# Kernel tuning notes

Hardware: AMD Instinct MI355X
Metric: run time of the kernel (lower is better)

## Reference

```python
import jax, jax.numpy as jnp
import numpy as np

MAX_ANGLES = 6
SCALES = 2
BN_EPS = 1e-5


def _gauss(k):
    # Gaussian filter init used by WaveletTransform1D (kernel_size k, sigma=k/4)
    xs = np.arange(k, dtype=np.float32) - k // 2
    w = np.exp(-xs ** 2 / (2.0 * (k / 4.0) ** 2)).astype(np.float32)
    return jnp.asarray((w / w.sum()).reshape(1, 1, k))


def setup_inputs():
    key = jax.random.key(0)
    ks = jax.random.split(key, 8)
    B, C, H, W = 8, 64, 128, 128
    return {
        "x": jax.random.normal(ks[0], (B, C, H, W), jnp.float32),
        "lin1_w": jax.random.normal(ks[1], (32, C * 16), jnp.float32) * 0.02,
        "lin1_b": jnp.zeros((32,), jnp.float32),
        "lin2_w": jax.random.normal(ks[2], (MAX_ANGLES, 32), jnp.float32) * 0.02,
        "lin2_b": jnp.zeros((MAX_ANGLES,), jnp.float32),
        "wf0": _gauss(3),
        "wf1": _gauss(5),
        "fuse_w": jax.random.normal(ks[3], (C, C * SCALES), jnp.float32) * 0.05,
        "fuse_b": jax.random.normal(ks[4], (C,), jnp.float32) * 0.05,
        "bn_gamma": jnp.ones((C,), jnp.float32),
        "bn_beta": jnp.zeros((C,), jnp.float32),
        "bn_mean": jnp.zeros((C,), jnp.float32),
        "bn_var": jnp.ones((C,), jnp.float32),
    }


def _grid_sample(img, grid):
    # torch F.grid_sample, bilinear, align_corners=True, padding_mode='zeros'
    N, C, H, W = img.shape
    ix = (grid[..., 0] + 1.0) * 0.5 * (W - 1)  # (N,Hg,Wg)
    iy = (grid[..., 1] + 1.0) * 0.5 * (H - 1)
    x0 = jnp.floor(ix)
    y0 = jnp.floor(iy)
    wx = ix - x0
    wy = iy - y0

    def gather(xi, yi):
        valid = (xi >= 0) & (xi <= W - 1) & (yi >= 0) & (yi <= H - 1)
        xc = jnp.clip(xi, 0, W - 1).astype(jnp.int32)
        yc = jnp.clip(yi, 0, H - 1).astype(jnp.int32)
        v = jax.vmap(lambda im, yy, xx: im[:, yy, xx])(img, yc, xc)  # (N,C,Hg,Wg)
        return v * valid[:, None, :, :].astype(img.dtype)

    v00 = gather(x0, y0)
    v01 = gather(x0 + 1, y0)
    v10 = gather(x0, y0 + 1)
    v11 = gather(x0 + 1, y0 + 1)
    return (v00 * ((1 - wx) * (1 - wy))[:, None]
            + v01 * (wx * (1 - wy))[:, None]
            + v10 * ((1 - wx) * wy)[:, None]
            + v11 * (wx * wy)[:, None])


def _interp1d(x, Lout):
    # F.interpolate mode='linear', align_corners=False, over last axis
    Lin = x.shape[-1]
    real = jnp.clip((jnp.arange(Lout, dtype=jnp.float32) + 0.5) * (Lin / Lout) - 0.5, 0.0, Lin - 1.0)
    i0 = jnp.floor(real).astype(jnp.int32)
    i1 = jnp.minimum(i0 + 1, Lin - 1)
    w = real - i0
    return x[..., i0] * (1.0 - w) + x[..., i1] * w


def _interp_last_ac(x, Lout):
    # linear interp over last axis, align_corners=True
    Lin = x.shape[-1]
    if Lin == Lout:
        return x
    pos = jnp.arange(Lout, dtype=jnp.float32) * ((Lin - 1) / (Lout - 1))
    i0 = jnp.floor(pos).astype(jnp.int32)
    i1 = jnp.minimum(i0 + 1, Lin - 1)
    w = pos - i0
    return x[..., i0] * (1.0 - w) + x[..., i1] * w


def _avgpool1(x):
    L = x.shape[-1]
    return x[..., : (L // 2) * 2].reshape(x.shape[:-1] + (L // 2, 2)).mean(-1)


def _conv1(sig, w):
    # sig (N,1,L), w (1,1,k), 'same' padding cross-correlation (matches torch Conv1d)
    k = w.shape[-1]
    return jax.lax.conv_general_dilated(sig, w, (1,), [(k // 2, k // 2)],
                                        dimension_numbers=("NCH", "OIH", "NCH"))


def reference(x, lin1_w, lin1_b, lin2_w, lin2_b, wf0, wf1, fuse_w, fuse_b,
              bn_gamma, bn_beta, bn_mean, bn_var):
    B, C, H, W = x.shape
    K = MAX_ANGLES
    # --- AnglePredictor: adaptive avg pool 4x4 (H,W divisible by 4) + MLP ---
    pooled = x.reshape(B, C, 4, H // 4, 4, W // 4).mean(axis=(3, 5))  # (B,C,4,4)
    feat = pooled.reshape(B, C * 16)
    h = jax.nn.relu(feat @ lin1_w.T + lin1_b)
    off = (h @ lin2_w.T + lin2_b) * 30.0
    base = jnp.linspace(0.0, 180.0, K)
    angles = jnp.sort(jnp.clip(base[None, :] + off, 0.0, 180.0), axis=1)  # (B,K)
    # --- RadonTransform: per-angle rotation grid + grid_sample + sum over W ---
    xs = jnp.linspace(-1.0, 1.0, W)
    ys = jnp.linspace(-1.0, 1.0, H)
    yc, xc = jnp.meshgrid(ys, xs, indexing="ij")
    th = angles * (jnp.pi / 180.0)
    co = jnp.cos(th)[:, :, None, None]
    si = jnp.sin(th)[:, :, None, None]
    gx = xc[None, None] * co + yc[None, None] * si
    gy = -xc[None, None] * si + yc[None, None] * co
    grid = jnp.stack([gx, gy], axis=-1).reshape(B * K, H, W, 2)
    xexp = jnp.broadcast_to(x[:, None], (B, K, C, H, W)).reshape(B * K, C, H, W)
    rotated = _grid_sample(xexp, grid)          # (B*K,C,H,W)
    sig = rotated.sum(axis=3)                   # (B*K,C,H) == sinogram permuted
    # --- WaveletTransform1D (2 scales, L=H=128 > 4) ---
    N = B * K
    c0 = _conv1(sig.reshape(N * C, 1, H), wf0).reshape(N, C, H)
    cur = _avgpool1(sig)                        # (N,C,H//2)
    L2 = H // 2
    f1 = _conv1(cur.reshape(N * C, 1, L2), wf1)
    u1 = _interp1d(_avgpool1(f1), L2).reshape(N, C, L2)
    c1 = _interp1d(u1, H)                       # resized to target length H
    coeffs = jnp.stack([c0, c1], axis=2)        # (N,C,SCALES,H)
    wav = coeffs.reshape(B, K, C, SCALES, H).transpose(0, 2, 4, 3, 1)  # (B,C,H,S,K)
    combined = wav.reshape(B, C * SCALES, H, K)  # matches torch .view on contiguous
    # --- bilinear align_corners=True resize (H,K)->(H,W), separable ---
    combined = _interp_last_ac(combined, W)
    combined = _interp_last_ac(combined.swapaxes(-1, -2), H).swapaxes(-1, -2)
    # --- fusion: 1x1 conv + BatchNorm(eval) + ReLU ---
    out = jnp.einsum("oc,bchw->bohw", fuse_w, combined) + fuse_b[None, :, None, None]
    scale = (bn_gamma / jnp.sqrt(bn_var + BN_EPS))[None, :, None, None]
    out = (out - bn_mean[None, :, None, None]) * scale + bn_beta[None, :, None, None]
    return jax.nn.relu(out)
```

## Files before the change

kernel.cpp:

```cpp
#include <hip/hip_runtime.h>
#include <math.h>

#define BB 8
#define CC 64
#define HH 128
#define WW 128
#define KK 6

#define FEAT_OFF 0
#define TH_OFF   8192
#define COEF_OFF 8256
#define S_OFF    (8256 + 786432)

__global__ __launch_bounds__(256) void k_pool(const float* __restrict__ x,
                                              float* __restrict__ ws) {
    int bc = blockIdx.x;
    int b = bc >> 6, c = bc & 63;
    int t = threadIdx.x;
    __shared__ float pool_l[16];
    if (t < 16) pool_l[t] = 0.f;
    __syncthreads();
    const float4* img4 = (const float4*)(x + (size_t)bc * 16384);
    float acc[4] = {0.f, 0.f, 0.f, 0.f};
    int cb = (t & 31) >> 3;
    #pragma unroll
    for (int r = 0; r < 16; ++r) {
        float4 v = img4[r * 256 + t];
        acc[r >> 2] += (v.x + v.y) + (v.z + v.w);
    }
    #pragma unroll
    for (int rb = 0; rb < 4; ++rb)
        atomicAdd(&pool_l[rb * 4 + cb], acc[rb]);
    __syncthreads();
    if (t < 16)
        ws[FEAT_OFF + b * 1024 + c * 16 + t] = pool_l[t] * (1.0f / 1024.0f);
}

__global__ __launch_bounds__(256) void k_mlp(const float* __restrict__ lin1_w,
                                             const float* __restrict__ lin1_b,
                                             const float* __restrict__ lin2_w,
                                             const float* __restrict__ lin2_b,
                                             float* __restrict__ ws) {
    int b = blockIdx.x;
    int t = threadIdx.x;
    __shared__ float feat_l[1024];
    __shared__ float h_l[32];
    __shared__ float ang_l[6];
    const float* feat = ws + FEAT_OFF + b * 1024;
    for (int i = t; i < 1024; i += 256) feat_l[i] = feat[i];
    __syncthreads();
    int m = t >> 3, part = t & 7;
    const float* wrow = lin1_w + m * 1024 + part * 128;
    const float* frow = feat_l + part * 128;
    float acc = 0.f;
    #pragma unroll 8
    for (int i = 0; i < 128; ++i) acc = fmaf(frow[i], wrow[i], acc);
    acc += __shfl_xor(acc, 1);
    acc += __shfl_xor(acc, 2);
    acc += __shfl_xor(acc, 4);
    if (part == 0) h_l[m] = fmaxf(acc + lin1_b[m], 0.f);
    __syncthreads();
    if (t < 6) {
        float a = lin2_b[t];
        #pragma unroll
        for (int i = 0; i < 32; ++i) a = fmaf(h_l[i], lin2_w[t * 32 + i], a);
        a = 36.0f * (float)t + a * 30.0f;
        ang_l[t] = fminf(fmaxf(a, 0.f), 180.f);
    }
    __syncthreads();
    if (t == 0) {
        float v[6];
        #pragma unroll
        for (int i = 0; i < 6; ++i) v[i] = ang_l[i];
        for (int i = 1; i < 6; ++i) {
            float key = v[i]; int j = i - 1;
            while (j >= 0 && v[j] > key) { v[j + 1] = v[j]; --j; }
            v[j + 1] = key;
        }
        #pragma unroll
        for (int i = 0; i < 6; ++i)
            ws[TH_OFF + b * 6 + i] = v[i] * (3.14159265358979323846f / 180.0f);
    }
}

__global__ __launch_bounds__(256) void k_radon(const float* __restrict__ x,
                                               const float* __restrict__ wf0,
                                               const float* __restrict__ wf1,
                                               float* __restrict__ ws) {
    int bc = blockIdx.x;
    int b = bc >> 6, c = bc & 63;
    int t = threadIdx.x;
    __shared__ float imgp[130 * 130];
    __shared__ float sigl[768];
    __shared__ float co_l[6], si_l[6];

    for (int i = t; i < 130; i += 256) {
        imgp[i] = 0.f;
        imgp[129 * 130 + i] = 0.f;
        imgp[i * 130] = 0.f;
        imgp[i * 130 + 129] = 0.f;
    }
    const float4* src4 = (const float4*)(x + (size_t)bc * 16384);
    for (int i = t; i < 4096; i += 256) {
        float4 v = src4[i];
        float* d = imgp + ((i >> 5) + 1) * 130 + ((i & 31) << 2) + 1;
        d[0] = v.x; d[1] = v.y; d[2] = v.z; d[3] = v.w;
    }
    if (t < 6) {
        float th = ws[TH_OFF + b * 6 + t];
        co_l[t] = cosf(th);
        si_l[t] = sinf(th);
    }
    __syncthreads();

    const float* base = imgp + 131;
    const float LO = -0.9999f, HIA = 127.9999f;

    for (int p = t; p < 768; p += 256) {
        int k = p >> 7, h = p & 127;
        float co = co_l[k], si = si_l[k];
        float yc = fmaf((float)h, 2.0f / 127.0f, -1.0f);
        float ix0 = (fmaf(yc, si, -co) + 1.0f) * 63.5f;
        float iy0 = (fmaf(yc, co,  si) + 1.0f) * 63.5f;

        float ic = 1.0f / co, is = 1.0f / (-si);
        float a1 = (LO - ix0) * ic, a2 = (HIA - ix0) * ic;
        float b1 = (LO - iy0) * is, b2 = (HIA - iy0) * is;
        float wlo = fmaxf(fmaxf(fminf(a1, a2), fminf(b1, b2)), 0.0f);
        float whi = fminf(fminf(fmaxf(a1, a2), fmaxf(b1, b2)), 127.0f);
        int wA = (int)ceilf(wlo);
        int wB = (int)floorf(whi) + 1;
        wA = max(0, min(wA, 128));
        wB = max(wA, min(wB, 128));
        while (wA < wB) {
            float ix = fmaf((float)wA, co, ix0), iy = fmaf((float)wA, -si, iy0);
            if (ix >= LO && ix <= HIA && iy >= LO && iy <= HIA) break;
            ++wA;
        }
        while (wB > wA) {
            float ix = fmaf((float)(wB - 1), co, ix0), iy = fmaf((float)(wB - 1), -si, iy0);
            if (ix >= LO && ix <= HIA && iy >= LO && iy <= HIA) break;
            --wB;
        }

        float acc = 0.f;
        for (int w = wA; w < wB; ++w) {
            float fw = (float)w;
            float ix = fmaf(fw,  co, ix0);
            float iy = fmaf(fw, -si, iy0);
            float xf = floorf(ix), yf = floorf(iy);
            float wx = ix - xf, wy = iy - yf;
            int x0 = (int)xf, y0 = (int)yf;
            const float* q = base + y0 * 130 + x0;
            float v00 = q[0], v01 = q[1];
            float v10 = q[130], v11 = q[131];
            float top = fmaf(wx, v01 - v00, v00);
            float bot = fmaf(wx, v11 - v10, v10);
            acc += fmaf(wy, bot - top, top);
        }
        sigl[p] = acc;
    }
    __syncthreads();

    float* cur = imgp;
    float* f1  = imgp + 384;
    float* p1  = imgp + 768;
    float* u1  = imgp + 960;
    float g0 = wf0[0], g1 = wf0[1], g2 = wf0[2];

    for (int p = t; p < 768; p += 256) {
        int k = p >> 7, h = p & 127;
        const float* s = sigl + k * 128;
        float sm1 = (h > 0)   ? s[h - 1] : 0.f;
        float sp1 = (h < 127) ? s[h + 1] : 0.f;
        float c0 = sm1 * g0 + s[h] * g1 + sp1 * g2;
        ws[COEF_OFF + (((b * 6 + k) * 64 + c) * 2 + 0) * 128 + h] = c0;
    }
    for (int q = t; q < 384; q += 256) {
        int k = q >> 6, l = q & 63;
        cur[q] = (sigl[k * 128 + 2 * l] + sigl[k * 128 + 2 * l + 1]) * 0.5f;
    }
    __syncthreads();

    float w10 = wf1[0], w11 = wf1[1], w12 = wf1[2], w13 = wf1[3], w14 = wf1[4];
    for (int q = t; q < 384; q += 256) {
        int k = q >> 6, l = q & 63;
        const float* cu = cur + k * 64;
        float a = cu[l] * w12;
        a += (l >= 2)  ? cu[l - 2] * w10 : 0.f;
        a += (l >= 1)  ? cu[l - 1] * w11 : 0.f;
        a += (l <= 62) ? cu[l + 1] * w13 : 0.f;
        a += (l <= 61) ? cu[l + 2] * w14 : 0.f;
        f1[q] = a;
    }
    __syncthreads();

    for (int q = t; q < 192; q += 256) {
        int k = q >> 5, m = q & 31;
        p1[q] = (f1[k * 64 + 2 * m] + f1[k * 64 + 2 * m + 1]) * 0.5f;
    }
    __syncthreads();

    for (int q = t; q < 384; q += 256) {
        int k = q >> 6, l = q & 63;
        float real = fminf(fmaxf(0.5f * (float)l - 0.25f, 0.f), 31.f);
        int i0 = (int)real;
        int i1 = min(i0 + 1, 31);
        float wv = real - (float)i0;
        u1[q] = p1[k * 32 + i0] * (1.f - wv) + p1[k * 32 + i1] * wv;
    }
    __syncthreads();

    for (int p = t; p < 768; p += 256) {
        int k = p >> 7, h = p & 127;
        float real = fminf(fmaxf(0.5f * (float)h - 0.25f, 0.f), 63.f);
        int i0 = (int)real;
        int i1 = min(i0 + 1, 63);
        float wv = real - (float)i0;
        float c1 = u1[k * 64 + i0] * (1.f - wv) + u1[k * 64 + i1] * wv;
        ws[COEF_OFF + (((b * 6 + k) * 64 + c) * 2 + 1) * 128 + h] = c1;
    }
}

__global__ __launch_bounds__(256) void k_fuse(const float* __restrict__ fuse_w,
                                              const float* __restrict__ fuse_b,
                                              const float* __restrict__ bn_gamma,
                                              const float* __restrict__ bn_beta,
                                              const float* __restrict__ bn_mean,
                                              const float* __restrict__ bn_var,
                                              float* __restrict__ ws) {
    int blk = blockIdx.x;
    int n = blk >> 2, q = blk & 3;
    int b = n / 6, k = n - b * 6;
    int t = threadIdx.x;
    __shared__ __align__(16) float M[128 * 128];
    __shared__ float w_l[16 * 128];
    const float* coef = ws + COEF_OFF + n * 16384;
    for (int i = t; i < 16384; i += 256) {
        int cc = i >> 8, rem = i & 255, s = rem >> 7, hpos = rem & 127;
        int c2 = 2 * cc + (hpos >> 6);
        int h2 = ((hpos & 63) << 1) | s;
        M[c2 * 128 + h2] = coef[i];
    }
    for (int i = t; i < 2048; i += 256)
        w_l[i] = fuse_w[(q * 16 + (i >> 7)) * 128 + (i & 127)];
    __syncthreads();

    int hg = t & 31;
    int og = t >> 5;
    float acc[2][4];
    #pragma unroll
    for (int oo = 0; oo < 2; ++oo)
        #pragma unroll
        for (int j = 0; j < 4; ++j) acc[oo][j] = 0.f;

    const float* w0 = w_l + (og * 2) * 128;
    const float* w1 = w0 + 128;
    for (int c2 = 0; c2 < 128; ++c2) {
        float4 m4 = *(const float4*)(M + c2 * 128 + (hg << 2));
        float a0 = w0[c2], a1 = w1[c2];
        acc[0][0] = fmaf(a0, m4.x, acc[0][0]);
        acc[0][1] = fmaf(a0, m4.y, acc[0][1]);
        acc[0][2] = fmaf(a0, m4.z, acc[0][2]);
        acc[0][3] = fmaf(a0, m4.w, acc[0][3]);
        acc[1][0] = fmaf(a1, m4.x, acc[1][0]);
        acc[1][1] = fmaf(a1, m4.y, acc[1][1]);
        acc[1][2] = fmaf(a1, m4.z, acc[1][2]);
        acc[1][3] = fmaf(a1, m4.w, acc[1][3]);
    }
    #pragma unroll
    for (int oo = 0; oo < 2; ++oo) {
        int o = q * 16 + og * 2 + oo;
        float scale = bn_gamma[o] * rsqrtf(bn_var[o] + 1e-5f);
        float shift = (fuse_b[o] - bn_mean[o]) * scale + bn_beta[o];
        int basei = ((b * 64 + o) * 128 + hg * 4) * 6 + k;
        #pragma unroll
        for (int j = 0; j < 4; ++j)
            ws[S_OFF + basei + j * 6] = fmaf(acc[oo][j], scale, shift);
    }
}

__global__ __launch_bounds__(256) void k_out(const float* __restrict__ S,
                                             float* __restrict__ out) {
    int idx = blockIdx.x * 256 + threadIdx.x;
    int w = idx & 127;
    int row = idx >> 7;
    float pos = (float)w * (5.0f / 127.0f);
    int i0 = min((int)pos, 5);
    int i1 = min(i0 + 1, 5);
    float tt = pos - (float)i0;
    const float* srow = S + row * 6;
    float val = srow[i0] * (1.f - tt) + srow[i1] * tt;
    out[idx] = fmaxf(val, 0.f);
}

extern "C" void kernel_launch(void* const* d_in, const int* in_sizes, int n_in,
                              void* d_out, int out_size, void* d_ws, size_t ws_size,
                              hipStream_t stream) {
    const float* x        = (const float*)d_in[0];
    const float* lin1_w   = (const float*)d_in[1];
    const float* lin1_b   = (const float*)d_in[2];
    const float* lin2_w   = (const float*)d_in[3];
    const float* lin2_b   = (const float*)d_in[4];
    const float* wf0      = (const float*)d_in[5];
    const float* wf1      = (const float*)d_in[6];
    const float* fuse_w   = (const float*)d_in[7];
    const float* fuse_b   = (const float*)d_in[8];
    const float* bn_gamma = (const float*)d_in[9];
    const float* bn_beta  = (const float*)d_in[10];
    const float* bn_mean  = (const float*)d_in[11];
    const float* bn_var   = (const float*)d_in[12];
    float* ws  = (float*)d_ws;
    float* out = (float*)d_out;

    hipLaunchKernelGGL(k_pool,  dim3(BB * CC), dim3(256), 0, stream, x, ws);
    hipLaunchKernelGGL(k_mlp,   dim3(BB),      dim3(256), 0, stream,
                       lin1_w, lin1_b, lin2_w, lin2_b, ws);
    hipLaunchKernelGGL(k_radon, dim3(BB * CC), dim3(256), 0, stream, x, wf0, wf1, ws);
    hipLaunchKernelGGL(k_fuse,  dim3(BB * KK * 4), dim3(256), 0, stream,
                       fuse_w, fuse_b, bn_gamma, bn_beta, bn_mean, bn_var, ws);
    hipLaunchKernelGGL(k_out,   dim3((BB * CC * HH * WW) / 256), dim3(256), 0, stream,
                       ws + S_OFF, out);
}
```

Before: 183.4 us.

## Add transposed LDS image copy and pick per-angle orientation to reduce bank conflicts

```diff
diff --git a/kernel.cpp b/kernel.cpp
--- a/kernel.cpp
+++ b/kernel.cpp
@@ -11,6 +11,14 @@
 #define TH_OFF   8192
 #define COEF_OFF 8256
 #define S_OFF    (8256 + 786432)
+
+#define STR  136
+#define NROW 132
+#define IMG_SZ (NROW * STR)
+#define N_OFF 0
+#define T_OFF IMG_SZ
+#define SIG_OFF (2 * IMG_SZ)
+#define LDS_TOT (2 * IMG_SZ + 768)
 
 __global__ __launch_bounds__(256) void k_pool(const float* __restrict__ x,
                                               float* __restrict__ ws) {
@@ -83,92 +91,119 @@
     }
 }
 
-__global__ __launch_bounds__(256) void k_radon(const float* __restrict__ x,
+__device__ __forceinline__ int sim_mult(float drift) {
+    unsigned c0 = 0, c1 = 0, c2 = 0, sat = 0;
+    for (int i = 0; i < 64; ++i) {
+        int bk = ((int)floorf(drift * (float)i + 0.5f)) & 31;
+        unsigned m = 1u << bk;
+        unsigned t0 = c0 & m;  c0 ^= m;
+        unsigned t1 = c1 & t0; c1 ^= t0;
+        unsigned t2 = c2 & t1; c2 ^= t1;
+        sat |= t2;
+    }
+    int best = 0;
+    for (int bk = 0; bk < 32; ++bk) {
+        int mm = ((c0 >> bk) & 1) | (((c1 >> bk) & 1) << 1)
+               | (((c2 >> bk) & 1) << 2) | (((sat >> bk) & 1) << 3);
+        best = max(best, mm);
+    }
+    return best;
+}
+
+__global__ __launch_bounds__(384) void k_radon(const float* __restrict__ x,
                                                const float* __restrict__ wf0,
                                                const float* __restrict__ wf1,
                                                float* __restrict__ ws) {
     int bc = blockIdx.x;
     int b = bc >> 6, c = bc & 63;
     int t = threadIdx.x;
-    __shared__ float imgp[130 * 130];
-    __shared__ float sigl[768];
+    __shared__ float S[LDS_TOT];
     __shared__ float co_l[6], si_l[6];
-
-    for (int i = t; i < 130; i += 256) {
-        imgp[i] = 0.f;
-        imgp[129 * 130 + i] = 0.f;
-        imgp[i * 130] = 0.f;
-        imgp[i * 130 + 129] = 0.f;
-    }
+    __shared__ int   sel_l[6];
+
+    for (int i = t; i < IMG_SZ; i += 384) S[N_OFF + i] = 0.f;
+    __syncthreads();
     const float4* src4 = (const float4*)(x + (size_t)bc * 16384);
-    for (int i = t; i < 4096; i += 256) {
+    for (int i = t; i < 4096; i += 384) {
         float4 v = src4[i];
-        float* d = imgp + ((i >> 5) + 1) * 130 + ((i & 31) << 2) + 1;
+        float* d = S + N_OFF + ((i >> 5) + 2) * STR + ((i & 31) << 2) + 2;
         d[0] = v.x; d[1] = v.y; d[2] = v.z; d[3] = v.w;
     }
     if (t < 6) {
         float th = ws[TH_OFF + b * 6 + t];
-        co_l[t] = cosf(th);
-        si_l[t] = sinf(th);
-    }
-    __syncthreads();
-
-    const float* base = imgp + 131;
-    const float LO = -0.9999f, HIA = 127.9999f;
-
-    for (int p = t; p < 768; p += 256) {
+        float co = cosf(th), si = sinf(th);
+        co_l[t] = co; si_l[t] = si;
+        int mN = sim_mult(fmaf(136.f, co, si));
+        int mT = sim_mult(fmaf(136.f, si, co));
+        sel_l[t] = (mT < mN) ? 1 : 0;
+    }
+    __syncthreads();
+    for (int j = t; j < NROW * NROW; j += 384) {
+        int yy = j / NROW, xx = j - yy * NROW;
+        S[T_OFF + xx * STR + yy] = S[N_OFF + yy * STR + xx];
+    }
+    __syncthreads();
+
+    #pragma unroll
+    for (int pass = 0; pass < 2; ++pass) {
+        int p = pass * 384 + t;
         int k = p >> 7, h = p & 127;
         float co = co_l[k], si = si_l[k];
+        int sel = sel_l[k];
         float yc = fmaf((float)h, 2.0f / 127.0f, -1.0f);
         float ix0 = (fmaf(yc, si, -co) + 1.0f) * 63.5f;
         float iy0 = (fmaf(yc, co,  si) + 1.0f) * 63.5f;
-
-        float ic = 1.0f / co, is = 1.0f / (-si);
-        float a1 = (LO - ix0) * ic, a2 = (HIA - ix0) * ic;
-        float b1 = (LO - iy0) * is, b2 = (HIA - iy0) * is;
-        float wlo = fmaxf(fmaxf(fminf(a1, a2), fminf(b1, b2)), 0.0f);
-        float whi = fminf(fminf(fmaxf(a1, a2), fmaxf(b1, b2)), 127.0f);
-        int wA = (int)ceilf(wlo);
-        int wB = (int)floorf(whi) + 1;
-        wA = max(0, min(wA, 128));
-        wB = max(wA, min(wB, 128));
-        while (wA < wB) {
-            float ix = fmaf((float)wA, co, ix0), iy = fmaf((float)wA, -si, iy0);
-            if (ix >= LO && ix <= HIA && iy >= LO && iy <= HIA) break;
-            ++wA;
+        float u0 = sel ? ix0 : iy0;
+        float v0 = sel ? iy0 : ix0;
+        float du = sel ? co  : -si;
+        float dv = sel ? -si : co;
+        int abase = (sel ? T_OFF : N_OFF) + 2 * STR + 2;
+
+        float idu = 1.0f / du, idv = 1.0f / dv;
+        float a1 = (-1.0f - u0) * idu, a2 = (128.0f - u0) * idu;
+        float b1 = (-1.0f - v0) * idv, b2 = (128.0f - v0) * idv;
+        float wlo = fmaxf(fminf(a1, a2), fminf(b1, b2));
+        float whi = fminf(fmaxf(a1, a2), fmaxf(b1, b2));
+        int wAl = min(max((int)floorf(wlo), 0), 128);
+        int wBl = min(max((int)ceilf(whi), 0), 127);
+        #pragma unroll
+        for (int sft = 1; sft < 64; sft <<= 1) {
+            wAl = min(wAl, __shfl_xor(wAl, sft));
+            wBl = max(wBl, __shfl_xor(wBl, sft));
         }
-        while (wB > wA) {
-            float ix = fmaf((float)(wB - 1), co, ix0), iy = fmaf((float)(wB - 1), -si, iy0);
-            if (ix >= LO && ix <= HIA && iy >= LO && iy <= HIA) break;
-            --wB;
+        int wA = max(wAl - 1, 0);
+        int wE = min(wBl + 2, 128);
+
+        float acc = 0.f;
+        #pragma unroll 2
+        for (int w = wA; w < wE; ++w) {
+            float fw = (float)w;
+            float u = fmaf(fw, du, u0);
+            float v = fmaf(fw, dv, v0);
+            float fu = floorf(u), fv = floorf(v);
+            float wu = u - fu, wv = v - fv;
+            int iu = (int)fu, iv = (int)fv;
+            iu = min(max(iu, -2), 128);
+            iv = min(max(iv, -2), 128);
+            int idx = abase + iu * STR + iv;
+            float q0 = S[idx],       q1 = S[idx + 1];
+            float q2 = S[idx + STR], q3 = S[idx + STR + 1];
+            float r0 = fmaf(wv, q1 - q0, q0);
+            float r1 = fmaf(wv, q3 - q2, q2);
+            acc += fmaf(wu, r1 - r0, r0);
         }
-
-        float acc = 0.f;
-        for (int w = wA; w < wB; ++w) {
-            float fw = (float)w;
-            float ix = fmaf(fw,  co, ix0);
-            float iy = fmaf(fw, -si, iy0);
-            float xf = floorf(ix), yf = floorf(iy);
-            float wx = ix - xf, wy = iy - yf;
-            int x0 = (int)xf, y0 = (int)yf;
-            const float* q = base + y0 * 130 + x0;
-            float v00 = q[0], v01 = q[1];
-            float v10 = q[130], v11 = q[131];
-            float top = fmaf(wx, v01 - v00, v00);
-            float bot = fmaf(wx, v11 - v10, v10);
-            acc += fmaf(wy, bot - top, top);
-        }
-        sigl[p] = acc;
-    }
-    __syncthreads();
-
-    float* cur = imgp;
-    float* f1  = imgp + 384;
-    float* p1  = imgp + 768;
-    float* u1  = imgp + 960;
+        S[SIG_OFF + p] = acc;
+    }
+    __syncthreads();
+
+    const float* sigl = S + SIG_OFF;
+    float* cur = S + N_OFF;
+    float* f1  = S + N_OFF + 384;
+    float* p1  = S + N_OFF + 768;
+    float* u1  = S + N_OFF + 960;
     float g0 = wf0[0], g1 = wf0[1], g2 = wf0[2];
 
-    for (int p = t; p < 768; p += 256) {
+    for (int p = t; p < 768; p += 384) {
         int k = p >> 7, h = p & 127;
         const float* s = sigl + k * 128;
         float sm1 = (h > 0)   ? s[h - 1] : 0.f;
@@ -176,14 +211,14 @@
         float c0 = sm1 * g0 + s[h] * g1 + sp1 * g2;
         ws[COEF_OFF + (((b * 6 + k) * 64 + c) * 2 + 0) * 128 + h] = c0;
     }
-    for (int q = t; q < 384; q += 256) {
+    for (int q = t; q < 384; q += 384) {
         int k = q >> 6, l = q & 63;
         cur[q] = (sigl[k * 128 + 2 * l] + sigl[k * 128 + 2 * l + 1]) * 0.5f;
     }
     __syncthreads();
 
     float w10 = wf1[0], w11 = wf1[1], w12 = wf1[2], w13 = wf1[3], w14 = wf1[4];
-    for (int q = t; q < 384; q += 256) {
+    for (int q = t; q < 384; q += 384) {
         int k = q >> 6, l = q & 63;
         const float* cu = cur + k * 64;
         float a = cu[l] * w12;
@@ -195,13 +230,13 @@
     }
     __syncthreads();
 
-    for (int q = t; q < 192; q += 256) {
+    for (int q = t; q < 192; q += 384) {
         int k = q >> 5, m = q & 31;
         p1[q] = (f1[k * 64 + 2 * m] + f1[k * 64 + 2 * m + 1]) * 0.5f;
     }
     __syncthreads();
 
-    for (int q = t; q < 384; q += 256) {
+    for (int q = t; q < 384; q += 384) {
         int k = q >> 6, l = q & 63;
         float real = fminf(fmaxf(0.5f * (float)l - 0.25f, 0.f), 31.f);
         int i0 = (int)real;
@@ -211,7 +246,7 @@
     }
     __syncthreads();
 
-    for (int p = t; p < 768; p += 256) {
+    for (int p = t; p < 768; p += 384) {
         int k = p >> 7, h = p & 127;
         float real = fminf(fmaxf(0.5f * (float)h - 0.25f, 0.f), 63.f);
         int i0 = (int)real;
@@ -280,7 +315,7 @@
     }
 }
 
-__global__ __launch_bounds__(256) void k_out(const float* __restrict__ S,
+__global__ __launch_bounds__(256) void k_out(const float* __restrict__ Sg,
                                              float* __restrict__ out) {
     int idx = blockIdx.x * 256 + threadIdx.x;
     int w = idx & 127;
@@ -289,7 +324,7 @@
     int i0 = min((int)pos, 5);
     int i1 = min(i0 + 1, 5);
     float tt = pos - (float)i0;
-    const float* srow = S + row * 6;
+    const float* srow = Sg + row * 6;
     float val = srow[i0] * (1.f - tt) + srow[i1] * tt;
     out[idx] = fmaxf(val, 0.f);
 }
@@ -316,7 +351,7 @@
     hipLaunchKernelGGL(k_pool,  dim3(BB * CC), dim3(256), 0, stream, x, ws);
     hipLaunchKernelGGL(k_mlp,   dim3(BB),      dim3(256), 0, stream,
                        lin1_w, lin1_b, lin2_w, lin2_b, ws);
-    hipLaunchKernelGGL(k_radon, dim3(BB * CC), dim3(256), 0, stream, x, wf0, wf1, ws);
+    hipLaunchKernelGGL(k_radon, dim3(BB * CC), dim3(384), 0, stream, x, wf0, wf1, ws);
     hipLaunchKernelGGL(k_fuse,  dim3(BB * KK * 4), dim3(256), 0, stream,
                        fuse_w, fuse_b, bn_gamma, bn_beta, bn_mean, bn_var, ws);
     hipLaunchKernelGGL(k_out,   dim3((BB * CC * HH * WW) / 256), dim3(256), 0, stream,
```

After: 211.0 us. +15.0%, slower.
